# Performance work log

Hardware: AMD Instinct MI355X
Metric: run time of the kernel (lower is better)

Reference implementation:

```python
import jax, jax.numpy as jnp
import numpy as np

NUM_HEADS = 8
BN_EPS = 1e-5  # torch BatchNorm default eps


def _bn(x, gamma, beta, mean, var, axis):
    """Inference-mode batch norm along `axis`."""
    shp = [1] * x.ndim
    shp[axis] = -1
    inv = (gamma / jnp.sqrt(var + BN_EPS)).reshape(shp)
    return (x - mean.reshape(shp)) * inv + beta.reshape(shp)


def setup_inputs() -> dict:
    key = jax.random.key(0)
    ks = jax.random.split(key, 10)
    B, C, H, W = 2, 128, 128, 128  # attended axis H == kernel_size == 128
    dh = C // NUM_HEADS            # 16
    x = jax.random.normal(ks[0], (B, C, H, W), jnp.float32)
    kqv_w = jax.random.normal(ks[1], (2 * C, C), jnp.float32) * (1.0 / np.sqrt(C))
    kqv_gamma = jax.random.uniform(ks[2], (2 * C,), jnp.float32, 0.5, 1.5)
    kqv_beta = jax.random.normal(ks[3], (2 * C,), jnp.float32) * 0.1
    kqv_mean = jax.random.normal(ks[4], (2 * C,), jnp.float32) * 0.1
    kqv_var = jax.random.uniform(ks[5], (2 * C,), jnp.float32, 0.5, 1.5)
    nh3 = 3 * NUM_HEADS
    logits_gamma = jax.random.uniform(ks[6], (nh3,), jnp.float32, 0.5, 1.5)
    logits_beta = jax.random.normal(ks[7], (nh3,), jnp.float32) * 0.1
    logits_mean = jax.random.normal(ks[8], (nh3,), jnp.float32) * 0.1
    logits_var = jax.random.uniform(ks[9], (nh3,), jnp.float32, 0.5, 1.5)
    rel_encoding = jax.random.normal(jax.random.fold_in(key, 99), (2 * dh, 2 * H - 1), jnp.float32)
    return {
        'x': x, 'kqv_w': kqv_w,
        'kqv_gamma': kqv_gamma, 'kqv_beta': kqv_beta, 'kqv_mean': kqv_mean, 'kqv_var': kqv_var,
        'logits_gamma': logits_gamma, 'logits_beta': logits_beta,
        'logits_mean': logits_mean, 'logits_var': logits_var,
        'rel_encoding': rel_encoding,
    }


def reference(x, kqv_w, kqv_gamma, kqv_beta, kqv_mean, kqv_var,
              logits_gamma, logits_beta, logits_mean, logits_var, rel_encoding):
    B, C, H, W = x.shape
    nh = NUM_HEADS
    dh = C // nh
    ksz = H  # kernel_size == attended axis (height_dim=True)

    # permute(0,3,1,2): (B,C,H,W) -> (B,W,C,H); fold width into batch
    xb = x.transpose(0, 3, 1, 2).reshape(B * W, C, H)

    # fused kqv 1x1 conv (bias-free) + BatchNorm1d
    kqv = jnp.einsum('oc,bch->boh', kqv_w, xb)  # (BW, 2C, H)
    kqv = _bn(kqv, kqv_gamma, kqv_beta, kqv_mean, kqv_var, axis=1)
    kqv = kqv.reshape(B * W, nh, 2 * dh, H)
    k = kqv[:, :, : dh // 2]          # (BW, nh, dh/2, H)
    q = kqv[:, :, dh // 2: dh]        # (BW, nh, dh/2, H)
    v = kqv[:, :, dh:]                # (BW, nh, dh,   H)

    # relative-position gather: rel_encoding[:, distance_matrix]
    idx = jnp.arange(ksz)
    dist = (idx[None, :] - idx[:, None] + ksz - 1).reshape(-1)  # (ksz*ksz,)
    rel = rel_encoding[:, dist].reshape(2 * dh, ksz, ksz)
    q_enc = rel[: dh // 2]
    k_enc = rel[dh // 2: dh]
    v_enc = rel[dh:]

    qk = jnp.einsum('bhdx,bhdy->bhxy', q, k)
    qr = jnp.einsum('bhdx,dxy->bhxy', q, q_enc)
    kr = jnp.einsum('bhdx,dxy->bhyx', k, k_enc)  # einsum + transpose(2,3) fused

    logits = jnp.concatenate([qk, qr, kr], axis=1)  # (BW, 3*nh, H, H)
    logits = _bn(logits, logits_gamma, logits_beta, logits_mean, logits_var, axis=1)
    logits = logits.reshape(B * W, 3, nh, H, H).sum(axis=1)
    weights = jax.nn.softmax(logits, axis=3)

    attn = jnp.einsum('bhxy,bhdy->bhdx', weights, v)
    attn_enc = jnp.einsum('bhxy,dxy->bhdx', weights, v_enc)
    # torch's cat(dim=-1)+reshape+sum(dim=-2) == elementwise sum of the two branches
    out = (attn + attn_enc).reshape(B, W, C, H)
    return out.transpose(0, 2, 3, 1)  # back to (B, C, H, W)
```

## Files before the change

### kernel.cpp

```cpp
#include <hip/hip_runtime.h>

typedef unsigned short u16;
typedef unsigned int u32;
typedef __attribute__((ext_vector_type(8))) unsigned short u16x8;
typedef __attribute__((ext_vector_type(8))) short s8v;
typedef _Float16 h8 __attribute__((ext_vector_type(8)));
typedef _Float16 h4 __attribute__((ext_vector_type(4)));
typedef __attribute__((ext_vector_type(4))) float f32x4;

__device__ __forceinline__ float b2f(u16 v) {
  union { unsigned int u; float f; } c; c.u = ((unsigned int)v) << 16; return c.f;
}
__device__ __forceinline__ u16 f2b(float f) {
  union { unsigned int u; float f; } c; c.f = f;
  unsigned int u = c.u;
  u += 0x7FFFu + ((u >> 16) & 1u);
  return (u16)(u >> 16);
}
__device__ __forceinline__ u32 packh2(float a, float b) {
  union { _Float16 h; u16 u; } ca, cb; ca.h = (_Float16)a; cb.h = (_Float16)b;
  return (u32)ca.u | ((u32)cb.u << 16);
}

__global__ __launch_bounds__(256) void prep_tables(
    const float* __restrict__ wmat, const float* __restrict__ rel,
    char* __restrict__ whi, char* __restrict__ wlo, char* __restrict__ relT) {
  int tid = threadIdx.x, blk = blockIdx.x;
  if (blk < 32) {
    int i = blk * 1024 + tid;
#pragma unroll
    for (int k = 0; k < 4; k++, i += 256) {
      float v = wmat[i];
      _Float16 h = (_Float16)v;
      ((_Float16*)whi)[i] = h;
      ((_Float16*)wlo)[i] = (_Float16)(v - (float)h);
    }
    return;
  }
  int r = tid;
  u16x8 qh, ql, kh, kl;
#pragma unroll
  for (int d = 0; d < 8; d++) {
    float vq = (r < 255) ? rel[d * 255 + r] : 0.f;
    u16 hb = f2b(vq); qh[d] = hb; ql[d] = f2b(vq - b2f(hb));
    float vk = (r < 255) ? rel[(8 + d) * 255 + r] : 0.f;
    hb = f2b(vk); kh[d] = hb; kl[d] = f2b(vk - b2f(hb));
  }
  ((u16x8*)(relT + 0))[r] = qh;
  ((u16x8*)(relT + 4096))[r] = ql;
  ((u16x8*)(relT + 8192))[r] = kh;
  ((u16x8*)(relT + 12288))[r] = kl;
#pragma unroll
  for (int d = 0; d < 16; d++) {
    float vv = (r < 255) ? rel[(16 + d) * 255 + r] : 0.f;
    *(_Float16*)(relT + 16384 + d * 512 + r * 2) = (_Float16)vv;
  }
}

__global__ __launch_bounds__(256) void transpose_x(
    const float* __restrict__ x, char* __restrict__ xt2) {
  __shared__ _Float16 tile[32][33];
  int z = blockIdx.z, b = z >> 7, h = z & 127;
  const float* s = x + (size_t)b * 2097152 + h * 128;
  int tx = threadIdx.x, ty = threadIdx.y;
  int c0 = blockIdx.y * 32, w0 = blockIdx.x * 32;
#pragma unroll
  for (int k = 0; k < 4; k++)
    tile[ty + k * 8][tx] = (_Float16)s[(size_t)(c0 + ty + k * 8) * 16384 + w0 + tx];
  __syncthreads();
#pragma unroll
  for (int k = 0; k < 4; k++) {
    int w = w0 + ty + k * 8;
    int n = b * 128 + w;
    int c = c0 + tx;
    *(_Float16*)(xt2 + (size_t)n * 32768 + h * 256 + ((((c >> 3) ^ (h & 7))) << 4) + (c & 7) * 2) =
        tile[tx][ty + k * 8];
  }
}

#define KQ_XS 0
#define KQ_FMT 16384
#define KQ_INV 33792
#define KQ_BIA 34816
#define LDS_K 35840
__global__ __launch_bounds__(256, 2) void kqv_mfma(
    const char* __restrict__ xt2, const char* __restrict__ whi, const char* __restrict__ wlo,
    const float* __restrict__ gam, const float* __restrict__ bet,
    const float* __restrict__ mea, const float* __restrict__ var,
    char* __restrict__ qkT, char* __restrict__ vT) {
  __shared__ __attribute__((aligned(16))) char sm[LDS_K];
  int tid = threadIdx.x;
  int h0 = 64 * blockIdx.x, n = blockIdx.y;
  int lane = tid & 63, wv = tid >> 6, g = lane >> 4, l15 = lane & 15;
  const char* src = xt2 + (size_t)n * 32768 + h0 * 256;
  for (int i = tid; i < 1024; i += 256)
    ((f32x4*)(sm + KQ_XS))[i] = ((const f32x4*)src)[i];
  {
    float gv = gam[tid], bb = bet[tid], mm = mea[tid], vv = var[tid];
    float inv = gv * rsqrtf(vv + 1e-5f);
    ((float*)(sm + KQ_INV))[tid] = inv;
    ((float*)(sm + KQ_BIA))[tid] = bb - mm * inv;
  }
  __syncthreads();
  f32x4 acc[4][4];
#pragma unroll
  for (int a = 0; a < 4; a++)
#pragma unroll
    for (int b = 0; b < 4; b++) acc[a][b] = (f32x4){0.f, 0.f, 0.f, 0.f};
  const char* wsel = (g & 1) ? wlo : whi;
  int cofs = (g >> 1) * 8;
#pragma unroll
  for (int kk = 0; kk < 8; kk++) {
    h8 af[4], bf[4];
#pragma unroll
    for (int tt = 0; tt < 4; tt++)
      af[tt] = *(const h8*)(wsel + (64 * wv + 16 * tt + l15) * 256 + (16 * kk + cofs) * 2);
#pragma unroll
    for (int ht = 0; ht < 4; ht++)
      bf[ht] = *(const h8*)(sm + KQ_XS + (16 * ht + l15) * 256 +
                            (((2 * kk + (g >> 1)) ^ (l15 & 7)) << 4));
#pragma unroll
    for (int tt = 0; tt < 4; tt++)
#pragma unroll
      for (int ht = 0; ht < 4; ht++)
        acc[tt][ht] = __builtin_amdgcn_mfma_f32_16x16x32_f16(af[tt], bf[ht], acc[tt][ht], 0, 0, 0);
  }
  for (int r = 0; r < 4; r++) {
    if (wv == r) {
#pragma unroll
      for (int tt = 0; tt < 4; tt++)
#pragma unroll
        for (int ht = 0; ht < 4; ht++) {
          int ob = 16 * tt + 4 * g;
#pragma unroll
          for (int i = 0; i < 4; i++) {
            int o = 64 * r + ob + i;
            float inv = ((float*)(sm + KQ_INV))[o];
            float bia = ((float*)(sm + KQ_BIA))[o];
            ((float*)(sm + KQ_FMT))[(ob + i) * 68 + 16 * ht + l15] = acc[tt][ht][i] * inv + bia;
          }
        }
    }
    __syncthreads();
    {
      int xl = tid & 63, hsel = (tid >> 6) & 1, kq = tid >> 7;
      int headi = 2 * r + hsel;
      int obl = hsel * 32 + kq * 8;
      u16x8 hi8, lo8;
#pragma unroll
      for (int d = 0; d < 8; d++) {
        float v = ((float*)(sm + KQ_FMT))[(obl + d) * 68 + xl];
        u16 hb = f2b(v);
        hi8[d] = hb;
        lo8[d] = f2b(v - b2f(hb));
      }
      char* dsth = qkT + (size_t)(n * 8 + headi) * 8192 + (kq * 2) * 2048 + (h0 + xl) * 16;
      *(u16x8*)dsth = hi8;
      *(u16x8*)(dsth + 2048) = lo8;
    }
    {
      int hsel = tid >> 7, d = (tid >> 3) & 15, xo = tid & 7;
      int headi = 2 * r + hsel;
      h8 vv;
#pragma unroll
      for (int j = 0; j < 8; j++)
        vv[j] = (_Float16)((float*)(sm + KQ_FMT))[(hsel * 32 + 16 + d) * 68 + xo * 8 + j];
      *(h8*)(vT + (size_t)(n * 8 + headi) * 4096 + d * 256 + (h0 + xo * 8) * 2) = vv;
    }
    __syncthreads();
  }
}

#define T1_STRIDE 592
#define T1_WAVE   9472
#define O_T2      37888
#define T2_STRIDE 296
#define T2_STRIP  4736
#define LDS_A     75776
__global__ __launch_bounds__(256, 2) void attn_mfma3(
    const char* __restrict__ qkT, const char* __restrict__ vT, const char* __restrict__ relT,
    const float* __restrict__ lg, const float* __restrict__ lb,
    const float* __restrict__ lm, const float* __restrict__ lv,
    _Float16* __restrict__ otmp) {
  __shared__ __attribute__((aligned(16))) char sm[LDS_A];
  const int tid = threadIdx.x;
  const int head = blockIdx.x, n = blockIdx.y;
  const int lane = tid & 63, wv = tid >> 6;
  const int g = lane >> 4, l15 = lane & 15;
  const char* qkb = qkT + (size_t)(n * 8 + head) * 8192;
  const char* vb = vT + (size_t)(n * 8 + head) * 4096;
  const char* kAp = qkb + ((g & 1) ? 2048 : 0);
  const char* qBp = qkb + 4096 + ((g >> 1) ? 2048 : 0);
  const char* kBp = qkb + ((g >> 1) ? 2048 : 0);
  const char* eqA = relT + ((g & 1) ? 4096 : 0);
  const char* ekA = relT + 8192 + ((g & 1) ? 4096 : 0);
  const char* veB = relT + 16384;

  float a0 = lg[head] * rsqrtf(lv[head] + 1e-5f);
  float a1 = lg[8 + head] * rsqrtf(lv[8 + head] + 1e-5f);
  float a2 = lg[16 + head] * rsqrtf(lv[16 + head] + 1e-5f);
  float bsum = (lb[head] - lm[head] * a0) + (lb[8 + head] - lm[8 + head] * a1) +
               (lb[16 + head] - lm[16 + head] * a2);

  const f32x4 zero4 = {0.f, 0.f, 0.f, 0.f};
  const int X0a = 32 * wv, X0b = X0a + 16;
  char* t1 = sm + wv * T1_WAVE;

  s8v qfA = *(const s8v*)(qBp + (X0a + l15) * 16);
  s8v qfB = *(const s8v*)(qBp + (X0b + l15) * 16);
  f32x4 s0[8], s1[8];
#pragma unroll
  for (int yt = 0; yt < 8; yt++) {
    s8v ka = *(const s8v*)(kAp + (yt * 16 + l15) * 16);
    f32x4 d0 = __builtin_amdgcn_mfma_f32_16x16x32_bf16(ka, qfA, zero4, 0, 0, 0);
    f32x4 d1 = __builtin_amdgcn_mfma_f32_16x16x32_bf16(ka, qfB, zero4, 0, 0, 0);
#pragma unroll
    for (int i = 0; i < 4; i++) {
      s0[yt][i] = a0 * d0[i] + bsum;
      s1[yt][i] = a0 * d1[i] + bsum;
    }
  }

  {
    s8v eqf[10];
    int rbu = 96 - X0a;
#pragma unroll
    for (int t = 0; t < 10; t++)
      eqf[t] = *(const s8v*)(eqA + (rbu + 16 * t + l15) * 16);
#pragma unroll
    for (int t = 0; t < 9; t++) {
      f32x4 d = __builtin_amdgcn_mfma_f32_16x16x32_bf16(eqf[t + 1], qfA, zero4, 0, 0, 0);
      *(f32x4*)(t1 + l15 * T1_STRIDE + (16 * t + 4 * g) * 4) = d;
    }
    {
      const float* r1p = (const float*)(t1 + l15 * T1_STRIDE) + (4 * g + 15 - l15);
#pragma unroll
      for (int yt = 0; yt < 8; yt++)
#pragma unroll
        for (int i = 0; i < 4; i++) s0[yt][i] += a1 * r1p[16 * yt + i];
    }
#pragma unroll
    for (int t = 0; t < 9; t++) {
      f32x4 d = __builtin_amdgcn_mfma_f32_16x16x32_bf16(eqf[t], qfB, zero4, 0, 0, 0);
      *(f32x4*)(t1 + l15 * T1_STRIDE + (16 * t + 4 * g) * 4) = d;
    }
    {
      const float* r1p = (const float*)(t1 + l15 * T1_STRIDE) + (4 * g + 15 - l15);
#pragma unroll
      for (int yt = 0; yt < 8; yt++)
#pragma unroll
        for (int i = 0; i < 4; i++) s1[yt][i] += a1 * r1p[16 * yt + i];
    }
  }

  {
    s8v ekf[10];
    int rbu2 = 96 - 32 * wv;
#pragma unroll
    for (int t = 0; t < 10; t++)
      ekf[t] = *(const s8v*)(ekA + (rbu2 + 16 * t + l15) * 16);
#pragma unroll
    for (int st = 0; st < 2; st++) {
      int Ys = 2 * wv + st;
      s8v kf = *(const s8v*)(kBp + (Ys * 16 + l15) * 16);
      char* t2 = sm + O_T2 + Ys * T2_STRIP;
#pragma unroll
      for (int t = 0; t < 9; t++) {
        f32x4 d = __builtin_amdgcn_mfma_f32_16x16x32_bf16(ekf[t + 1 - st], kf, zero4, 0, 0, 0);
        h4 hv;
#pragma unroll
        for (int i = 0; i < 4; i++) hv[i] = (_Float16)d[i];
        *(h4*)(t2 + l15 * T2_STRIDE + (16 * t + 4 * g) * 2) = hv;
      }
    }
  }
  __syncthreads();

#pragma unroll
  for (int ir = 0; ir < 4; ir++) {
    const char* b2 = sm + O_T2 + (4 * g + ir) * T2_STRIDE + (X0a + l15 + 15 - 4 * g - ir) * 2;
#pragma unroll
    for (int yt = 0; yt < 8; yt++) {
      float v0 = (float)*(const _Float16*)(b2 + yt * T2_STRIP);
      float v1 = (float)*(const _Float16*)(b2 + yt * T2_STRIP + 32);
      s0[yt][ir] += a2 * v0;
      s1[yt][ir] += a2 * v1;
    }
  }

  float rl0, rl1;
  {
    float m0 = -1e30f, m1 = -1e30f;
#pragma unroll
    for (int yt = 0; yt < 8; yt++)
#pragma unroll
      for (int i = 0; i < 4; i++) {
        m0 = fmaxf(m0, s0[yt][i]);
        m1 = fmaxf(m1, s1[yt][i]);
      }
    m0 = fmaxf(m0, __shfl_xor(m0, 16)); m0 = fmaxf(m0, __shfl_xor(m0, 32));
    m1 = fmaxf(m1, __shfl_xor(m1, 16)); m1 = fmaxf(m1, __shfl_xor(m1, 32));
    float l0 = 0.f, l1 = 0.f;
#pragma unroll
    for (int yt = 0; yt < 8; yt++)
#pragma unroll
      for (int i = 0; i < 4; i++) {
        float p0 = __expf(s0[yt][i] - m0); s0[yt][i] = p0; l0 += p0;
        float p1 = __expf(s1[yt][i] - m1); s1[yt][i] = p1; l1 += p1;
      }
    l0 += __shfl_xor(l0, 16); l0 += __shfl_xor(l0, 32);
    l1 += __shfl_xor(l1, 16); l1 += __shfl_xor(l1, 32);
    rl0 = 1.f / l0; rl1 = 1.f / l1;
  }

  u32 ppk0[8][2], ppk1[8][2];
#pragma unroll
  for (int yt = 0; yt < 8; yt++) {
    ppk0[yt][0] = packh2(s0[yt][0], s0[yt][1]);
    ppk0[yt][1] = packh2(s0[yt][2], s0[yt][3]);
    ppk1[yt][0] = packh2(s1[yt][0], s1[yt][1]);
    ppk1[yt][1] = packh2(s1[yt][2], s1[yt][3]);
  }

  f32x4 acc0 = zero4, acc1 = zero4;
  {
    int addrA = ((2 * (g & 1)) * 16 + l15) * 4;
    int addrB = addrA + 64;
    bool hi = (g >> 1) != 0;
#pragma unroll
    for (int ky = 0; ky < 4; ky++) {
      h8 vf = *(const h8*)(vb + l15 * 256 + (32 * ky + 8 * g) * 2);
      union { u32 w[4]; h8 v; } pa, pb;
#pragma unroll
      for (int p = 0; p < 2; p++) {
        u32 e0a = __builtin_amdgcn_ds_bpermute(addrA, (int)ppk0[2 * ky][p]);
        u32 e1a = __builtin_amdgcn_ds_bpermute(addrA, (int)ppk0[2 * ky + 1][p]);
        u32 e0b = __builtin_amdgcn_ds_bpermute(addrB, (int)ppk0[2 * ky][p]);
        u32 e1b = __builtin_amdgcn_ds_bpermute(addrB, (int)ppk0[2 * ky + 1][p]);
        pa.w[p] = hi ? e1a : e0a;
        pa.w[p + 2] = hi ? e1b : e0b;
        u32 f0a = __builtin_amdgcn_ds_bpermute(addrA, (int)ppk1[2 * ky][p]);
        u32 f1a = __builtin_amdgcn_ds_bpermute(addrA, (int)ppk1[2 * ky + 1][p]);
        u32 f0b = __builtin_amdgcn_ds_bpermute(addrB, (int)ppk1[2 * ky][p]);
        u32 f1b = __builtin_amdgcn_ds_bpermute(addrB, (int)ppk1[2 * ky + 1][p]);
        pb.w[p] = hi ? f1a : f0a;
        pb.w[p + 2] = hi ? f1b : f0b;
      }
      acc0 = __builtin_amdgcn_mfma_f32_16x16x32_f16(vf, pa.v, acc0, 0, 0, 0);
      acc1 = __builtin_amdgcn_mfma_f32_16x16x32_f16(vf, pb.v, acc1, 0, 0, 0);
    }
  }

  {
    char* skb0 = t1;
    char* skb1 = t1 + 1280;
    for (int i = lane; i < 160; i += 64) *(f32x4*)(t1 + i * 16) = zero4;
    h8 vef[9];
#pragma unroll
    for (int u = 0; u < 9; u++)
      vef[u] = *(const h8*)(veB + l15 * 512 + ((96 - X0a + 16 * u) + 8 * g) * 2);
    int j0 = 4 * g + 15 - l15;
#pragma unroll
    for (int Ys = 0; Ys < 8; Ys++) {
      {
        u32 pk0 = ppk0[Ys][0], pk1 = ppk0[Ys][1];
        char* rp = skb0 + l15 * 80;
        *(u16*)(rp + (j0 + 0) * 2) = (u16)(pk0 & 0xffff);
        *(u16*)(rp + (j0 + 1) * 2) = (u16)(pk0 >> 16);
        *(u16*)(rp + (j0 + 2) * 2) = (u16)(pk1 & 0xffff);
        *(u16*)(rp + (j0 + 3) * 2) = (u16)(pk1 >> 16);
        h8 skf = *(const h8*)(skb0 + l15 * 80 + g * 16);
        acc0 = __builtin_amdgcn_mfma_f32_16x16x32_f16(vef[Ys + 1], skf, acc0, 0, 0, 0);
      }
      {
        u32 pk0 = ppk1[Ys][0], pk1 = ppk1[Ys][1];
        char* rp = skb1 + l15 * 80;
        *(u16*)(rp + (j0 + 0) * 2) = (u16)(pk0 & 0xffff);
        *(u16*)(rp + (j0 + 1) * 2) = (u16)(pk0 >> 16);
        *(u16*)(rp + (j0 + 2) * 2) = (u16)(pk1 & 0xffff);
        *(u16*)(rp + (j0 + 3) * 2) = (u16)(pk1 >> 16);
        h8 skf = *(const h8*)(skb1 + l15 * 80 + g * 16);
        acc1 = __builtin_amdgcn_mfma_f32_16x16x32_f16(vef[Ys], skf, acc1, 0, 0, 0);
      }
    }
  }

  size_t obase = (size_t)(n * 8 + head) * 2048;
#pragma unroll
  for (int i = 0; i < 4; i++) {
    int d = 4 * g + i;
    otmp[obase + d * 128 + X0a + l15] = (_Float16)(acc0[i] * rl0);
    otmp[obase + d * 128 + X0b + l15] = (_Float16)(acc1[i] * rl1);
  }
}

__global__ __launch_bounds__(256) void transpose_h2f(
    const u16* __restrict__ src, float* __restrict__ dst,
    int sb, int sc, int sstr, int db, int dc, int dstr) {
  __shared__ u16 tile[32][33];
  int z = blockIdx.z, b = z >> 7, c = z & 127;
  const u16* s = src + (size_t)b * sb + c * sc;
  float* d = dst + (size_t)b * db + c * dc;
  int tx = threadIdx.x, ty = threadIdx.y;
  int r0 = blockIdx.y * 32, c0 = blockIdx.x * 32;
#pragma unroll
  for (int k = 0; k < 4; k++)
    tile[ty + k * 8][tx] = s[(size_t)(r0 + ty + k * 8) * sstr + c0 + tx];
  __syncthreads();
#pragma unroll
  for (int k = 0; k < 4; k++) {
    u16 hv = tile[tx][ty + k * 8];
    d[(size_t)(c0 + ty + k * 8) * dstr + r0 + tx] = (float)(*(const _Float16*)&hv);
  }
}

extern "C" void kernel_launch(void* const* d_in, const int* in_sizes, int n_in,
                              void* d_out, int out_size, void* d_ws, size_t ws_size,
                              hipStream_t stream) {
  const float* x     = (const float*)d_in[0];
  const float* kqv_w = (const float*)d_in[1];
  const float* kqv_g = (const float*)d_in[2];
  const float* kqv_b = (const float*)d_in[3];
  const float* kqv_m = (const float*)d_in[4];
  const float* kqv_v = (const float*)d_in[5];
  const float* lg    = (const float*)d_in[6];
  const float* lb    = (const float*)d_in[7];
  const float* lm    = (const float*)d_in[8];
  const float* lv    = (const float*)d_in[9];
  const float* rel   = (const float*)d_in[10];
  float* out = (float*)d_out;

  char* ws = (char*)d_ws;
  char* xt2  = ws;
  char* qkT  = ws + 8388608;
  char* vT   = ws + 25165824;
  _Float16* otmp = (_Float16*)(ws + 33554432);
  char* whi  = ws + 41943040;
  char* wlo  = ws + 42008576;
  char* relT = ws + 42074112;

  prep_tables<<<33, 256, 0, stream>>>(kqv_w, rel, whi, wlo, relT);
  transpose_x<<<dim3(4, 4, 256), dim3(32, 8), 0, stream>>>(x, xt2);
  kqv_mfma<<<dim3(2, 256), 256, 0, stream>>>(xt2, whi, wlo, kqv_g, kqv_b, kqv_m, kqv_v, qkT, vT);
  attn_mfma3<<<dim3(8, 256), 256, 0, stream>>>(qkT, vT, relT, lg, lb, lm, lv, otmp);
  transpose_h2f<<<dim3(4, 4, 256), dim3(32, 8), 0, stream>>>(
      (const u16*)otmp, out, 2097152, 128, 16384, 2097152, 16384, 128);
}
```

Before: 85.54 us.

## Restructure attention kernel to per-wave LDS scratch for higher occupancy

Shared memory drops to a per-wave scratch region, removing the block-wide kr strip buffer and its __syncthreads. Launch bounds rise from 2 to 4 blocks per CU. The kr relative term is now computed in small per-yt chunks that are consumed right away. The P·V operand exchange uses LDS stores and loads instead of many ds_bpermute calls, and the v_enc term uses a wider skewed LDS row with fewer MFMAs. The aim is more occupancy and less register pressure, at the cost of recomputing some ekf fragments and adding more LDS round trips.

Result: faster. 80.67 us (-5.7%).

```diff
diff --git a/kernel.cpp b/kernel.cpp
--- a/kernel.cpp
+++ b/kernel.cpp
@@ -21,6 +21,9 @@
   union { _Float16 h; u16 u; } ca, cb; ca.h = (_Float16)a; cb.h = (_Float16)b;
   return (u32)ca.u | ((u32)cb.u << 16);
 }
+__device__ __forceinline__ u16 f2h_bits(float a) {
+  union { _Float16 h; u16 u; } c; c.h = (_Float16)a; return c.u;
+}
 
 __global__ __launch_bounds__(256) void prep_tables(
     const float* __restrict__ wmat, const float* __restrict__ rel,
@@ -53,7 +56,8 @@
 #pragma unroll
   for (int d = 0; d < 16; d++) {
     float vv = (r < 255) ? rel[(16 + d) * 255 + r] : 0.f;
-    *(_Float16*)(relT + 16384 + d * 512 + r * 2) = (_Float16)vv;
+    *(_Float16*)(relT + 16384 + d * 1024 + r * 2) = (_Float16)vv;
+    *(_Float16*)(relT + 16384 + d * 1024 + (256 + r) * 2) = (_Float16)0.f;
   }
 }
 
@@ -171,13 +175,10 @@
   }
 }
 
+#define SW_BYTES 9472
 #define T1_STRIDE 592
-#define T1_WAVE   9472
-#define O_T2      37888
-#define T2_STRIDE 296
-#define T2_STRIP  4736
-#define LDS_A     75776
-__global__ __launch_bounds__(256, 2) void attn_mfma3(
+#define LDS_A 37888
+__global__ __launch_bounds__(256, 4) void attn_mfma4(
     const char* __restrict__ qkT, const char* __restrict__ vT, const char* __restrict__ relT,
     const float* __restrict__ lg, const float* __restrict__ lb,
     const float* __restrict__ lm, const float* __restrict__ lv,
@@ -187,11 +188,12 @@
   const int head = blockIdx.x, n = blockIdx.y;
   const int lane = tid & 63, wv = tid >> 6;
   const int g = lane >> 4, l15 = lane & 15;
+  char* sw = sm + wv * SW_BYTES;
   const char* qkb = qkT + (size_t)(n * 8 + head) * 8192;
   const char* vb = vT + (size_t)(n * 8 + head) * 4096;
   const char* kAp = qkb + ((g & 1) ? 2048 : 0);
+  const char* kBp = qkb + ((g >> 1) ? 2048 : 0);
   const char* qBp = qkb + 4096 + ((g >> 1) ? 2048 : 0);
-  const char* kBp = qkb + ((g >> 1) ? 2048 : 0);
   const char* eqA = relT + ((g & 1) ? 4096 : 0);
   const char* ekA = relT + 8192 + ((g & 1) ? 4096 : 0);
   const char* veB = relT + 16384;
@@ -204,7 +206,6 @@
 
   const f32x4 zero4 = {0.f, 0.f, 0.f, 0.f};
   const int X0a = 32 * wv, X0b = X0a + 16;
-  char* t1 = sm + wv * T1_WAVE;
 
   s8v qfA = *(const s8v*)(qBp + (X0a + l15) * 16);
   s8v qfB = *(const s8v*)(qBp + (X0b + l15) * 16);
@@ -230,10 +231,10 @@
 #pragma unroll
     for (int t = 0; t < 9; t++) {
       f32x4 d = __builtin_amdgcn_mfma_f32_16x16x32_bf16(eqf[t + 1], qfA, zero4, 0, 0, 0);
-      *(f32x4*)(t1 + l15 * T1_STRIDE + (16 * t + 4 * g) * 4) = d;
+      *(f32x4*)(sw + l15 * T1_STRIDE + (16 * t + 4 * g) * 4) = d;
     }
     {
-      const float* r1p = (const float*)(t1 + l15 * T1_STRIDE) + (4 * g + 15 - l15);
+      const float* r1p = (const float*)(sw + l15 * T1_STRIDE) + (4 * g + 15 - l15);
 #pragma unroll
       for (int yt = 0; yt < 8; yt++)
 #pragma unroll
@@ -242,10 +243,10 @@
 #pragma unroll
     for (int t = 0; t < 9; t++) {
       f32x4 d = __builtin_amdgcn_mfma_f32_16x16x32_bf16(eqf[t], qfB, zero4, 0, 0, 0);
-      *(f32x4*)(t1 + l15 * T1_STRIDE + (16 * t + 4 * g) * 4) = d;
+      *(f32x4*)(sw + l15 * T1_STRIDE + (16 * t + 4 * g) * 4) = d;
     }
     {
-      const float* r1p = (const float*)(t1 + l15 * T1_STRIDE) + (4 * g + 15 - l15);
+      const float* r1p = (const float*)(sw + l15 * T1_STRIDE) + (4 * g + 15 - l15);
 #pragma unroll
       for (int yt = 0; yt < 8; yt++)
 #pragma unroll
@@ -253,38 +254,36 @@
     }
   }
 
-  {
-    s8v ekf[10];
-    int rbu2 = 96 - 32 * wv;
-#pragma unroll
-    for (int t = 0; t < 10; t++)
-      ekf[t] = *(const s8v*)(ekA + (rbu2 + 16 * t + l15) * 16);
-#pragma unroll
-    for (int st = 0; st < 2; st++) {
-      int Ys = 2 * wv + st;
-      s8v kf = *(const s8v*)(kBp + (Ys * 16 + l15) * 16);
-      char* t2 = sm + O_T2 + Ys * T2_STRIP;
-#pragma unroll
-      for (int t = 0; t < 9; t++) {
-        f32x4 d = __builtin_amdgcn_mfma_f32_16x16x32_bf16(ekf[t + 1 - st], kf, zero4, 0, 0, 0);
+#pragma unroll
+  for (int grp = 0; grp < 2; grp++) {
+#pragma unroll
+    for (int q4 = 0; q4 < 4; q4++) {
+      int yt = grp * 4 + q4;
+      int rb2 = X0a - 16 * yt + 112;
+      char* buf = sw + q4 * 1664;
+      s8v kf = *(const s8v*)(kBp + (16 * yt + l15) * 16);
+#pragma unroll
+      for (int t = 0; t < 3; t++) {
+        s8v ef = *(const s8v*)(ekA + (rb2 + 16 * t + l15) * 16);
+        f32x4 d = __builtin_amdgcn_mfma_f32_16x16x32_bf16(ef, kf, zero4, 0, 0, 0);
         h4 hv;
 #pragma unroll
         for (int i = 0; i < 4; i++) hv[i] = (_Float16)d[i];
-        *(h4*)(t2 + l15 * T2_STRIDE + (16 * t + 4 * g) * 2) = hv;
-      }
-    }
-  }
-  __syncthreads();
-
-#pragma unroll
-  for (int ir = 0; ir < 4; ir++) {
-    const char* b2 = sm + O_T2 + (4 * g + ir) * T2_STRIDE + (X0a + l15 + 15 - 4 * g - ir) * 2;
-#pragma unroll
-    for (int yt = 0; yt < 8; yt++) {
-      float v0 = (float)*(const _Float16*)(b2 + yt * T2_STRIP);
-      float v1 = (float)*(const _Float16*)(b2 + yt * T2_STRIP + 32);
-      s0[yt][ir] += a2 * v0;
-      s1[yt][ir] += a2 * v1;
+        *(h4*)(buf + l15 * 104 + (16 * t + 4 * g) * 2) = hv;
+      }
+    }
+#pragma unroll
+    for (int q4 = 0; q4 < 4; q4++) {
+      int yt = grp * 4 + q4;
+      const char* buf = sw + q4 * 1664;
+#pragma unroll
+      for (int i = 0; i < 4; i++) {
+        const char* bp = buf + (4 * g + i) * 104 + (l15 + 15 - 4 * g - i) * 2;
+        float v0 = (float)*(const _Float16*)bp;
+        float v1 = (float)*(const _Float16*)(bp + 32);
+        s0[yt][i] += a2 * v0;
+        s1[yt][i] += a2 * v1;
+      }
     }
   }
 
@@ -313,75 +312,56 @@
     rl0 = 1.f / l0; rl1 = 1.f / l1;
   }
 
-  u32 ppk0[8][2], ppk1[8][2];
 #pragma unroll
   for (int yt = 0; yt < 8; yt++) {
-    ppk0[yt][0] = packh2(s0[yt][0], s0[yt][1]);
-    ppk0[yt][1] = packh2(s0[yt][2], s0[yt][3]);
-    ppk1[yt][0] = packh2(s1[yt][0], s1[yt][1]);
-    ppk1[yt][1] = packh2(s1[yt][2], s1[yt][3]);
-  }
-
+    char* pa = sw + l15 * 272 + (16 * yt + 4 * g) * 2;
+    *(u32*)pa = packh2(s0[yt][0], s0[yt][1]);
+    *(u32*)(pa + 4) = packh2(s0[yt][2], s0[yt][3]);
+    char* pb = sw + (16 + l15) * 272 + (16 * yt + 4 * g) * 2;
+    *(u32*)pb = packh2(s1[yt][0], s1[yt][1]);
+    *(u32*)(pb + 4) = packh2(s1[yt][2], s1[yt][3]);
+  }
   f32x4 acc0 = zero4, acc1 = zero4;
+#pragma unroll
+  for (int ky = 0; ky < 4; ky++) {
+    h8 vf = *(const h8*)(vb + l15 * 256 + (32 * ky + 8 * g) * 2);
+    h8 p0 = *(const h8*)(sw + l15 * 272 + (32 * ky + 8 * g) * 2);
+    h8 p1 = *(const h8*)(sw + (16 + l15) * 272 + (32 * ky + 8 * g) * 2);
+    acc0 = __builtin_amdgcn_mfma_f32_16x16x32_f16(vf, p0, acc0, 0, 0, 0);
+    acc1 = __builtin_amdgcn_mfma_f32_16x16x32_f16(vf, p1, acc1, 0, 0, 0);
+  }
+
+  for (int i = lane; i < 336; i += 64) *(f32x4*)(sw + i * 16) = zero4;
   {
-    int addrA = ((2 * (g & 1)) * 16 + l15) * 4;
-    int addrB = addrA + 64;
-    bool hi = (g >> 1) != 0;
-#pragma unroll
-    for (int ky = 0; ky < 4; ky++) {
-      h8 vf = *(const h8*)(vb + l15 * 256 + (32 * ky + 8 * g) * 2);
-      union { u32 w[4]; h8 v; } pa, pb;
-#pragma unroll
-      for (int p = 0; p < 2; p++) {
-        u32 e0a = __builtin_amdgcn_ds_bpermute(addrA, (int)ppk0[2 * ky][p]);
-        u32 e1a = __builtin_amdgcn_ds_bpermute(addrA, (int)ppk0[2 * ky + 1][p]);
-        u32 e0b = __builtin_amdgcn_ds_bpermute(addrB, (int)ppk0[2 * ky][p]);
-        u32 e1b = __builtin_amdgcn_ds_bpermute(addrB, (int)ppk0[2 * ky + 1][p]);
-        pa.w[p] = hi ? e1a : e0a;
-        pa.w[p + 2] = hi ? e1b : e0b;
-        u32 f0a = __builtin_amdgcn_ds_bpermute(addrA, (int)ppk1[2 * ky][p]);
-        u32 f1a = __builtin_amdgcn_ds_bpermute(addrA, (int)ppk1[2 * ky + 1][p]);
-        u32 f0b = __builtin_amdgcn_ds_bpermute(addrB, (int)ppk1[2 * ky][p]);
-        u32 f1b = __builtin_amdgcn_ds_bpermute(addrB, (int)ppk1[2 * ky + 1][p]);
-        pb.w[p] = hi ? f1a : f0a;
-        pb.w[p + 2] = hi ? f1b : f0b;
-      }
-      acc0 = __builtin_amdgcn_mfma_f32_16x16x32_f16(vf, pa.v, acc0, 0, 0, 0);
-      acc1 = __builtin_amdgcn_mfma_f32_16x16x32_f16(vf, pb.v, acc1, 0, 0, 0);
-    }
-  }
-
+#pragma unroll
+    for (int yt = 0; yt < 8; yt++)
+#pragma unroll
+      for (int i = 0; i < 4; i++) {
+        int col = 16 * yt + 4 * g + i - l15 + 15;
+        *(u16*)(sw + l15 * 336 + col * 2) = f2h_bits(s0[yt][i]);
+      }
+    int rb_a = 112 - X0a;
+#pragma unroll
+    for (int t = 0; t < 5; t++) {
+      h8 vef = *(const h8*)(veB + l15 * 1024 + (rb_a + 32 * t + 8 * g) * 2);
+      h8 skf = *(const h8*)(sw + l15 * 336 + (32 * t + 8 * g) * 2);
+      acc0 = __builtin_amdgcn_mfma_f32_16x16x32_f16(vef, skf, acc0, 0, 0, 0);
+    }
+  }
   {
-    char* skb0 = t1;
-    char* skb1 = t1 + 1280;
-    for (int i = lane; i < 160; i += 64) *(f32x4*)(t1 + i * 16) = zero4;
-    h8 vef[9];
-#pragma unroll
-    for (int u = 0; u < 9; u++)
-      vef[u] = *(const h8*)(veB + l15 * 512 + ((96 - X0a + 16 * u) + 8 * g) * 2);
-    int j0 = 4 * g + 15 - l15;
-#pragma unroll
-    for (int Ys = 0; Ys < 8; Ys++) {
-      {
-        u32 pk0 = ppk0[Ys][0], pk1 = ppk0[Ys][1];
-        char* rp = skb0 + l15 * 80;
-        *(u16*)(rp + (j0 + 0) * 2) = (u16)(pk0 & 0xffff);
-        *(u16*)(rp + (j0 + 1) * 2) = (u16)(pk0 >> 16);
-        *(u16*)(rp + (j0 + 2) * 2) = (u16)(pk1 & 0xffff);
-        *(u16*)(rp + (j0 + 3) * 2) = (u16)(pk1 >> 16);
-        h8 skf = *(const h8*)(skb0 + l15 * 80 + g * 16);
-        acc0 = __builtin_amdgcn_mfma_f32_16x16x32_f16(vef[Ys + 1], skf, acc0, 0, 0, 0);
-      }
-      {
-        u32 pk0 = ppk1[Ys][0], pk1 = ppk1[Ys][1];
-        char* rp = skb1 + l15 * 80;
-        *(u16*)(rp + (j0 + 0) * 2) = (u16)(pk0 & 0xffff);
-        *(u16*)(rp + (j0 + 1) * 2) = (u16)(pk0 >> 16);
-        *(u16*)(rp + (j0 + 2) * 2) = (u16)(pk1 & 0xffff);
-        *(u16*)(rp + (j0 + 3) * 2) = (u16)(pk1 >> 16);
-        h8 skf = *(const h8*)(skb1 + l15 * 80 + g * 16);
-        acc1 = __builtin_amdgcn_mfma_f32_16x16x32_f16(vef[Ys], skf, acc1, 0, 0, 0);
-      }
+#pragma unroll
+    for (int yt = 0; yt < 8; yt++)
+#pragma unroll
+      for (int i = 0; i < 4; i++) {
+        int col = 16 * yt + 4 * g + i - l15 + 15;
+        *(u16*)(sw + l15 * 336 + col * 2) = f2h_bits(s1[yt][i]);
+      }
+    int rb_b = 96 - X0a;
+#pragma unroll
+    for (int t = 0; t < 5; t++) {
+      h8 vef = *(const h8*)(veB + l15 * 1024 + (rb_b + 32 * t + 8 * g) * 2);
+      h8 skf = *(const h8*)(sw + l15 * 336 + (32 * t + 8 * g) * 2);
+      acc1 = __builtin_amdgcn_mfma_f32_16x16x32_f16(vef, skf, acc1, 0, 0, 0);
     }
   }
 
@@ -442,7 +422,7 @@
   prep_tables<<<33, 256, 0, stream>>>(kqv_w, rel, whi, wlo, relT);
   transpose_x<<<dim3(4, 4, 256), dim3(32, 8), 0, stream>>>(x, xt2);
   kqv_mfma<<<dim3(2, 256), 256, 0, stream>>>(xt2, whi, wlo, kqv_g, kqv_b, kqv_m, kqv_v, qkT, vT);
-  attn_mfma3<<<dim3(8, 256), 256, 0, stream>>>(qkT, vT, relT, lg, lb, lm, lv, otmp);
+  attn_mfma4<<<dim3(8, 256), 256, 0, stream>>>(qkT, vT, relT, lg, lb, lm, lv, otmp);
   transpose_h2f<<<dim3(4, 4, 256), dim3(32, 8), 0, stream>>>(
       (const u16*)otmp, out, 2097152, 128, 16384, 2097152, 16384, 128);
 }
```
